# Optimization experiments

Measured on AMD Instinct MI355X. Metric: run time of the kernel, lower is better.

The kernel has to match this reference:

```python
import jax, jax.numpy as jnp
import numpy as np

LOSS_WEIGHT = 1.0


def _norm_gram(feat):
    # feat: [B, C, H, W] -> normalized channel gram [B, C, C]
    B, C, H, W = feat.shape
    F = feat.reshape(B, C, H * W)                      # [B, C, HW]
    gram = jnp.einsum('bcn,bdn->bcd', F, F)            # [B, C, C]
    n = jnp.sqrt(jnp.sum(F * F, axis=2))               # [B, C] per-channel L2 norm
    norm_M = n[:, :, None] * n[:, None, :]             # [B, C, C]
    return gram / norm_M


def setup_inputs() -> dict:
    key = jax.random.key(0)
    k1, k2 = jax.random.split(key)
    det = jax.random.normal(k1, (8, 512, 128, 128), dtype=jnp.float32)
    sr = jax.random.normal(k2, (8, 512, 128, 128), dtype=jnp.float32)
    return {"det": det, "sr": sr}


def reference(det, sr):
    sm_det = _norm_gram(det)
    sm_sr = _norm_gram(sr)
    # use_l2=True -> MSELoss (mean reduction); weighted_loss with weight=None,
    # reduction='mean' on a scalar is identity; then * loss_weight.
    loss = jnp.mean((sm_det - sm_sr) ** 2)
    return loss * LOSS_WEIGHT
```

## Files before the change

kernel.cpp:

```cpp
#include <hip/hip_runtime.h>
#include <hip/hip_bf16.h>

#define C_CH 512
#define HW 16384
#define NB 8
#define TILE 128
#define BK 64
#define NTB 4
#define NTILES 10
#define KSPLIT 8
#define KCHUNK (HW / KSPLIT)
#define KSTEPS (KCHUNK / BK)
#define NGRAM 16
#define CC (C_CH * C_CH)
#define LOSS_BLOCKS 1024

typedef float f32x4 __attribute__((ext_vector_type(4)));
typedef float f32x8 __attribute__((ext_vector_type(8)));
typedef __bf16 bf16x8 __attribute__((ext_vector_type(8)));

__global__ __launch_bounds__(256) void gram_kernel(const float* __restrict__ det,
                                                   const float* __restrict__ sr,
                                                   float* __restrict__ gram) {
    const int tid = threadIdx.x;
    int bid = blockIdx.x;
    const int ks = bid & (KSPLIT - 1);
    bid >>= 3;
    const int t = bid % NTILES;
    const int g = bid / NTILES;
    const int tensor = g >> 3, b = g & 7;

    int ti = 0, tt = t;
    while (tt >= NTB - ti) { tt -= NTB - ti; ++ti; }
    const int tj = ti + tt;
    const bool diag = (ti == tj);

    const float* F = (tensor ? sr : det) + (size_t)b * C_CH * HW;
    const int k0 = ks * KCHUNK;
    const float* Abase = F + (size_t)(ti * TILE) * HW + k0;
    const float* Bbase = F + (size_t)(tj * TILE) * HW + k0;

    __shared__ bf16x8 As8[TILE * BK / 8];
    __shared__ bf16x8 Bs8[TILE * BK / 8];
    __bf16* As = (__bf16*)As8;
    __bf16* Bs = (__bf16*)Bs8;

    const int lane = tid & 63;
    const int w = tid >> 6;
    const int wr = w >> 1, wc = w & 1;

    f32x4 acc[4][4] = {};

    for (int kt = 0; kt < KSTEPS; ++kt) {
        const int koff = kt * BK;
        __syncthreads();
        #pragma unroll
        for (int q = 0; q < 4; ++q) {
            int c = q * 256 + tid;
            int row = c >> 3, ch = c & 7;
            f32x8 v = *(const f32x8*)(Abase + (size_t)row * HW + koff + ch * 8);
            bf16x8 h;
            #pragma unroll
            for (int i = 0; i < 8; ++i) h[i] = (__bf16)v[i];
            *(bf16x8*)(As + row * BK + ((ch ^ (row & 7)) << 3)) = h;
        }
        if (!diag) {
            #pragma unroll
            for (int q = 0; q < 4; ++q) {
                int c = q * 256 + tid;
                int row = c >> 3, ch = c & 7;
                f32x8 v = *(const f32x8*)(Bbase + (size_t)row * HW + koff + ch * 8);
                bf16x8 h;
                #pragma unroll
                for (int i = 0; i < 8; ++i) h[i] = (__bf16)v[i];
                *(bf16x8*)(Bs + row * BK + ((ch ^ (row & 7)) << 3)) = h;
            }
        }
        __syncthreads();
        const __bf16* Bsrc = diag ? As : Bs;
        #pragma unroll
        for (int ksub = 0; ksub < 2; ++ksub) {
            const int kchunk = ksub * 4 + (lane >> 4);
            bf16x8 af[4], bfr[4];
            #pragma unroll
            for (int m = 0; m < 4; ++m) {
                int row = wr * 64 + m * 16 + (lane & 15);
                af[m] = *(const bf16x8*)(As + row * BK + ((kchunk ^ (row & 7)) << 3));
            }
            #pragma unroll
            for (int n = 0; n < 4; ++n) {
                int row = wc * 64 + n * 16 + (lane & 15);
                bfr[n] = *(const bf16x8*)(Bsrc + row * BK + ((kchunk ^ (row & 7)) << 3));
            }
            #pragma unroll
            for (int m = 0; m < 4; ++m)
                #pragma unroll
                for (int n = 0; n < 4; ++n)
                    acc[m][n] = __builtin_amdgcn_mfma_f32_16x16x32_bf16(af[m], bfr[n], acc[m][n], 0, 0, 0);
        }
    }

    float* gout = gram + (size_t)g * CC;
    const int rbase = ti * TILE + wr * 64 + ((lane >> 4) << 2);
    const int cbase = tj * TILE + wc * 64 + (lane & 15);
    #pragma unroll
    for (int m = 0; m < 4; ++m)
        #pragma unroll
        for (int n = 0; n < 4; ++n)
            #pragma unroll
            for (int j = 0; j < 4; ++j)
                atomicAdd(&gout[(size_t)(rbase + m * 16 + j) * C_CH + cbase + n * 16], acc[m][n][j]);
}

__global__ void norm_kernel(const float* __restrict__ gram, float* __restrict__ invn) {
    const int g = blockIdx.x, c = threadIdx.x;
    float v = gram[(size_t)g * CC + (size_t)c * C_CH + c];
    invn[g * C_CH + c] = 1.0f / sqrtf(v);
}

__global__ __launch_bounds__(256) void loss_kernel(const float* __restrict__ gram,
                                                   const float* __restrict__ invn,
                                                   float* __restrict__ partials) {
    const int tid = threadIdx.x;
    float s = 0.f;
    for (int idx = blockIdx.x * 256 + tid; idx < NB * CC; idx += LOSS_BLOCKS * 256) {
        int b = idx >> 18;
        int c = (idx >> 9) & 511;
        int d = idx & 511;
        int cc = c, dd = d;
        if ((dd >> 7) < (cc >> 7)) { int tmp = cc; cc = dd; dd = tmp; }
        float gd = gram[(size_t)b * CC + (size_t)cc * C_CH + dd];
        float gs = gram[(size_t)(8 + b) * CC + (size_t)cc * C_CH + dd];
        float sd = gd * invn[b * C_CH + c] * invn[b * C_CH + d];
        float ss = gs * invn[(8 + b) * C_CH + c] * invn[(8 + b) * C_CH + d];
        float diff = sd - ss;
        s += diff * diff;
    }
    #pragma unroll
    for (int off = 32; off > 0; off >>= 1) s += __shfl_down(s, off, 64);
    __shared__ float red[4];
    if ((tid & 63) == 0) red[tid >> 6] = s;
    __syncthreads();
    if (tid == 0) partials[blockIdx.x] = red[0] + red[1] + red[2] + red[3];
}

__global__ void final_kernel(const float* __restrict__ partials, float* __restrict__ out) {
    const int tid = threadIdx.x;
    float s = 0.f;
    for (int i = tid; i < LOSS_BLOCKS; i += 256) s += partials[i];
    #pragma unroll
    for (int off = 32; off > 0; off >>= 1) s += __shfl_down(s, off, 64);
    __shared__ float red[4];
    if ((tid & 63) == 0) red[tid >> 6] = s;
    __syncthreads();
    if (tid == 0) out[0] = (red[0] + red[1] + red[2] + red[3]) * (1.0f / (float)(NB * (size_t)CC));
}

extern "C" void kernel_launch(void* const* d_in, const int* in_sizes, int n_in,
                              void* d_out, int out_size, void* d_ws, size_t ws_size,
                              hipStream_t stream) {
    const float* det = (const float*)d_in[0];
    const float* sr  = (const float*)d_in[1];
    float* gram     = (float*)d_ws;
    float* invn     = gram + (size_t)NGRAM * CC;
    float* partials = invn + NGRAM * C_CH;
    float* out      = (float*)d_out;

    hipMemsetAsync(gram, 0, (size_t)NGRAM * CC * sizeof(float), stream);
    gram_kernel<<<NGRAM * NTILES * KSPLIT, 256, 0, stream>>>(det, sr, gram);
    norm_kernel<<<NGRAM, C_CH, 0, stream>>>(gram, invn);
    loss_kernel<<<LOSS_BLOCKS, 256, 0, stream>>>(gram, invn, partials);
    final_kernel<<<1, 256, 0, stream>>>(partials, out);
}
```

Before: 265.9 us.

## Use 256x256 gram tiles with register-prefetch double buffering and triangular diagonal skip

Gram tiles grow from 128 to 256 channels, leaving 3 upper-triangular tiles per batch instead of 10. The K split rises to 16, and blocks grow to 512 threads with a block-index swizzle. The main loop prefetches the next K slice into registers and double-buffers LDS, so global loads overlap MFMA work. Diagonal tiles skip MFMAs and atomics for sub-blocks wholly below the diagonal, and the loss kernel now mirrors every element with d<c. This cuts redundant global reads of the input and wasted compute, at the cost of higher register pressure (acc[8][4] plus prefetch registers) and fewer, heavier blocks.

```diff
diff --git a/kernel.cpp b/kernel.cpp
--- a/kernel.cpp
+++ b/kernel.cpp
@@ -4,112 +4,137 @@
 #define C_CH 512
 #define HW 16384
 #define NB 8
-#define TILE 128
+#define TILE 256
 #define BK 64
-#define NTB 4
-#define NTILES 10
-#define KSPLIT 8
+#define NTILES 3
+#define KSPLIT 16
 #define KCHUNK (HW / KSPLIT)
 #define KSTEPS (KCHUNK / BK)
 #define NGRAM 16
 #define CC (C_CH * C_CH)
 #define LOSS_BLOCKS 1024
+#define GRID (NGRAM * NTILES * KSPLIT)
+#define PANEL_V8 (TILE * BK / 8)
 
 typedef float f32x4 __attribute__((ext_vector_type(4)));
 typedef float f32x8 __attribute__((ext_vector_type(8)));
 typedef __bf16 bf16x8 __attribute__((ext_vector_type(8)));
 
-__global__ __launch_bounds__(256) void gram_kernel(const float* __restrict__ det,
-                                                   const float* __restrict__ sr,
-                                                   float* __restrict__ gram) {
-    const int tid = threadIdx.x;
-    int bid = blockIdx.x;
-    const int ks = bid & (KSPLIT - 1);
-    bid >>= 3;
-    const int t = bid % NTILES;
-    const int g = bid / NTILES;
+__global__ __launch_bounds__(512, 2) void gram_kernel(const float* __restrict__ det,
+                                                      const float* __restrict__ sr,
+                                                      float* __restrict__ gram) {
+    const int lbid = ((int)blockIdx.x & 7) * (GRID / 8) + (int)blockIdx.x / 8;
+    const int t = lbid % NTILES;
+    const int gk = lbid / NTILES;
+    const int ks = gk & (KSPLIT - 1);
+    const int g = gk >> 4;
     const int tensor = g >> 3, b = g & 7;
-
-    int ti = 0, tt = t;
-    while (tt >= NTB - ti) { tt -= NTB - ti; ++ti; }
-    const int tj = ti + tt;
-    const bool diag = (ti == tj);
+    const int ti = (t == 2) ? 1 : 0;
+    const int tj = (t == 0) ? 0 : 1;
+    const bool diag = (t != 1);
 
     const float* F = (tensor ? sr : det) + (size_t)b * C_CH * HW;
-    const int k0 = ks * KCHUNK;
-    const float* Abase = F + (size_t)(ti * TILE) * HW + k0;
-    const float* Bbase = F + (size_t)(tj * TILE) * HW + k0;
+    const float* Abase = F + (size_t)(ti * TILE) * HW + ks * KCHUNK;
+    const float* Bbase = F + (size_t)(tj * TILE) * HW + ks * KCHUNK;
 
-    __shared__ bf16x8 As8[TILE * BK / 8];
-    __shared__ bf16x8 Bs8[TILE * BK / 8];
-    __bf16* As = (__bf16*)As8;
-    __bf16* Bs = (__bf16*)Bs8;
+    __shared__ bf16x8 lds[4 * PANEL_V8];
 
+    const int tid = threadIdx.x;
     const int lane = tid & 63;
-    const int w = tid >> 6;
-    const int wr = w >> 1, wc = w & 1;
+    const int wid = tid >> 6;
+    const int wr = wid >> 2, wc = wid & 3;
 
-    f32x4 acc[4][4] = {};
+    int goff[4], lofs[4];
+    #pragma unroll
+    for (int q = 0; q < 4; ++q) {
+        int c = q * 512 + tid;
+        int row = c >> 3, ch = c & 7;
+        goff[q] = row * HW + ch * 8;
+        lofs[q] = row * (BK / 8) + (ch ^ (row & 7));
+    }
 
-    for (int kt = 0; kt < KSTEPS; ++kt) {
-        const int koff = kt * BK;
-        __syncthreads();
+    f32x8 va[4], vb[4];
+    auto LOAD = [&](int kt) {
+        const int ko = kt * BK;
+        #pragma unroll
+        for (int q = 0; q < 4; ++q) va[q] = *(const f32x8*)(Abase + goff[q] + ko);
+        if (!diag) {
+            #pragma unroll
+            for (int q = 0; q < 4; ++q) vb[q] = *(const f32x8*)(Bbase + goff[q] + ko);
+        }
+    };
+    auto WRITE = [&](int buf) {
+        bf16x8* As = lds + buf * 2 * PANEL_V8;
         #pragma unroll
         for (int q = 0; q < 4; ++q) {
-            int c = q * 256 + tid;
-            int row = c >> 3, ch = c & 7;
-            f32x8 v = *(const f32x8*)(Abase + (size_t)row * HW + koff + ch * 8);
             bf16x8 h;
             #pragma unroll
-            for (int i = 0; i < 8; ++i) h[i] = (__bf16)v[i];
-            *(bf16x8*)(As + row * BK + ((ch ^ (row & 7)) << 3)) = h;
+            for (int i = 0; i < 8; ++i) h[i] = (__bf16)va[q][i];
+            As[lofs[q]] = h;
         }
         if (!diag) {
+            bf16x8* Bs = As + PANEL_V8;
             #pragma unroll
             for (int q = 0; q < 4; ++q) {
-                int c = q * 256 + tid;
-                int row = c >> 3, ch = c & 7;
-                f32x8 v = *(const f32x8*)(Bbase + (size_t)row * HW + koff + ch * 8);
                 bf16x8 h;
                 #pragma unroll
-                for (int i = 0; i < 8; ++i) h[i] = (__bf16)v[i];
-                *(bf16x8*)(Bs + row * BK + ((ch ^ (row & 7)) << 3)) = h;
+                for (int i = 0; i < 8; ++i) h[i] = (__bf16)vb[q][i];
+                Bs[lofs[q]] = h;
             }
         }
-        __syncthreads();
-        const __bf16* Bsrc = diag ? As : Bs;
+    };
+
+    f32x4 acc[8][4] = {};
+    auto COMPUTE = [&](int buf) {
+        const __bf16* As = (const __bf16*)(lds + buf * 2 * PANEL_V8);
+        const __bf16* Bs = diag ? As : As + PANEL_V8 * 8;
         #pragma unroll
         for (int ksub = 0; ksub < 2; ++ksub) {
             const int kchunk = ksub * 4 + (lane >> 4);
-            bf16x8 af[4], bfr[4];
+            bf16x8 af[8], bfr[4];
             #pragma unroll
-            for (int m = 0; m < 4; ++m) {
-                int row = wr * 64 + m * 16 + (lane & 15);
+            for (int m = 0; m < 8; ++m) {
+                int row = wr * 128 + m * 16 + (lane & 15);
                 af[m] = *(const bf16x8*)(As + row * BK + ((kchunk ^ (row & 7)) << 3));
             }
             #pragma unroll
             for (int n = 0; n < 4; ++n) {
                 int row = wc * 64 + n * 16 + (lane & 15);
-                bfr[n] = *(const bf16x8*)(Bsrc + row * BK + ((kchunk ^ (row & 7)) << 3));
+                bfr[n] = *(const bf16x8*)(Bs + row * BK + ((kchunk ^ (row & 7)) << 3));
             }
             #pragma unroll
-            for (int m = 0; m < 4; ++m)
+            for (int m = 0; m < 8; ++m)
                 #pragma unroll
                 for (int n = 0; n < 4; ++n)
-                    acc[m][n] = __builtin_amdgcn_mfma_f32_16x16x32_bf16(af[m], bfr[n], acc[m][n], 0, 0, 0);
+                    if (!diag || (wc * 64 + n * 16 + 16 > wr * 128 + m * 16))
+                        acc[m][n] = __builtin_amdgcn_mfma_f32_16x16x32_bf16(af[m], bfr[n], acc[m][n], 0, 0, 0);
         }
+    };
+
+    LOAD(0);
+    WRITE(0);
+    __syncthreads();
+    int cur = 0;
+    for (int kt = 0; kt < KSTEPS; ++kt) {
+        if (kt + 1 < KSTEPS) LOAD(kt + 1);
+        COMPUTE(cur);
+        if (kt + 1 < KSTEPS) WRITE(cur ^ 1);
+        __syncthreads();
+        cur ^= 1;
     }
 
     float* gout = gram + (size_t)g * CC;
-    const int rbase = ti * TILE + wr * 64 + ((lane >> 4) << 2);
-    const int cbase = tj * TILE + wc * 64 + (lane & 15);
+    const int rb = ti * TILE + wr * 128 + ((lane >> 4) << 2);
+    const int cb = tj * TILE + wc * 64 + (lane & 15);
     #pragma unroll
-    for (int m = 0; m < 4; ++m)
+    for (int m = 0; m < 8; ++m)
         #pragma unroll
-        for (int n = 0; n < 4; ++n)
+        for (int n = 0; n < 4; ++n) {
+            if (diag && (wc * 64 + n * 16 + 16 <= wr * 128 + m * 16)) continue;
             #pragma unroll
             for (int j = 0; j < 4; ++j)
-                atomicAdd(&gout[(size_t)(rbase + m * 16 + j) * C_CH + cbase + n * 16], acc[m][n][j]);
+                atomicAdd(&gout[(size_t)(rb + m * 16 + j) * C_CH + cb + n * 16], acc[m][n][j]);
+        }
 }
 
 __global__ void norm_kernel(const float* __restrict__ gram, float* __restrict__ invn) {
@@ -128,7 +153,7 @@
         int c = (idx >> 9) & 511;
         int d = idx & 511;
         int cc = c, dd = d;
-        if ((dd >> 7) < (cc >> 7)) { int tmp = cc; cc = dd; dd = tmp; }
+        if (dd < cc) { int tmp = cc; cc = dd; dd = tmp; }
         float gd = gram[(size_t)b * CC + (size_t)cc * C_CH + dd];
         float gs = gram[(size_t)(8 + b) * CC + (size_t)cc * C_CH + dd];
         float sd = gd * invn[b * C_CH + c] * invn[b * C_CH + d];
@@ -167,7 +192,7 @@
     float* out      = (float*)d_out;
 
     hipMemsetAsync(gram, 0, (size_t)NGRAM * CC * sizeof(float), stream);
-    gram_kernel<<<NGRAM * NTILES * KSPLIT, 256, 0, stream>>>(det, sr, gram);
+    gram_kernel<<<GRID, 512, 0, stream>>>(det, sr, gram);
     norm_kernel<<<NGRAM, C_CH, 0, stream>>>(gram, invn);
     loss_kernel<<<LOSS_BLOCKS, 256, 0, stream>>>(gram, invn, partials);
     final_kernel<<<1, 256, 0, stream>>>(partials, out);
```

New measurement: 374.6 us. 1.41x slower.
